# Optimization experiments

Hardware: AMD Instinct MI355X
Metric: run time of the kernel (lower is better)

## Reference

```python
import jax, jax.numpy as jnp
import numpy as np

NE, NM, D = 10000, 2048, 128
LEVELS = 6  # levels arg 5 -> self.levels = 6 relation types


def setup_inputs() -> dict:
    key = jax.random.key(0)
    ks = jax.random.split(key, 9)
    s = 0.05
    return {
        "emb_entity": jax.random.normal(ks[0], (1, NE, D), jnp.float32),
        "emb_mole": jax.random.normal(ks[1], (1, NM, D), jnp.float32),
        "entity_mole_weight": jax.random.uniform(ks[2], (NE, NM), jnp.float32),
        "W1": jax.random.normal(ks[3], (LEVELS, D, D), jnp.float32) * s,
        "root1": jax.random.normal(ks[4], (D, D), jnp.float32) * s,
        "b1": jax.random.normal(ks[5], (D,), jnp.float32) * s,
        "W2": jax.random.normal(ks[6], (LEVELS, D, D), jnp.float32) * s,
        "root2": jax.random.normal(ks[7], (D, D), jnp.float32) * s,
        "b2": jax.random.normal(ks[8], (D,), jnp.float32) * s,
    }


def reference(emb_entity, emb_mole, entity_mole_weight, W1, root1, b1, W2, root2, b2):
    x_e = emb_entity[0]  # [NE, D]
    x_m = emb_mole[0]    # [NM, D]
    # weight w in (i/LEVELS, (i+1)/LEVELS]  <=>  ceil(w*LEVELS) - 1 == i ; only i=1..LEVELS-1 form edges
    lev = jnp.ceil(entity_mole_weight * LEVELS).astype(jnp.int32) - 1  # [NE, NM]

    def rel_agg(x_src, W):
        # RGCN mean aggregation per relation type (edges Mole -> Entity), summed over relations
        out = jnp.zeros((x_e.shape[0], W.shape[-1]), x_src.dtype)
        for r in range(1, LEVELS):
            mask = (lev == r).astype(x_src.dtype)          # [NE, NM] relation-r adjacency
            cnt = mask.sum(axis=1, keepdims=True)          # in-degree per entity for relation r
            inv = jnp.where(cnt > 0, 1.0 / cnt, 0.0)
            out = out + ((mask @ x_src) * inv) @ W[r]      # mean message then relation transform
        return out

    # conv1 over homogeneous graph [Entity; Mole]; moles receive no edges -> root+bias only
    e1 = x_e @ root1 + rel_agg(x_m, W1) + b1
    m1 = x_m @ root1 + b1
    e1 = jax.nn.relu(e1)
    m1 = jax.nn.relu(m1)
    # conv2; only the entity slice of the output is returned
    e2 = e1 @ root2 + rel_agg(m1, W2) + b2
    return e2[None]  # [1, NE, D]
```

## Files before the change

### kernel.cpp

```cpp
#include <hip/hip_runtime.h>
#include <stdint.h>


#define NE 10000
#define NM 2048
#define NEPAD 10112
#define MB128 79
#define KSPLIT 16

typedef short bf8_t __attribute__((ext_vector_type(8)));
typedef float f16f  __attribute__((ext_vector_type(16)));

__device__ __forceinline__ uint16_t f2bf(float f){
  uint32_t u = __float_as_uint(f);
  u += 0x7FFFu + ((u >> 16) & 1u);
  return (uint16_t)(u >> 16);
}

__device__ __forceinline__ f16f mfma32(bf8_t a, bf8_t b, f16f c){
  return __builtin_amdgcn_mfma_f32_32x32x16_bf16(a, b, c, 0, 0, 0);
}

__global__ __launch_bounds__(256) void k_init(
    const float* __restrict__ root1, const float* __restrict__ root2,
    const float* __restrict__ W1, const float* __restrict__ W2,
    uint16_t* __restrict__ r1t, uint16_t* __restrict__ r2t,
    uint16_t* __restrict__ w1t, uint16_t* __restrict__ w2t,
    const float* __restrict__ w, const float* __restrict__ xe,
    uint32_t* __restrict__ levq, float* __restrict__ inv,
    uint16_t* __restrict__ xebf){
  int t = threadIdx.x;
  if (blockIdx.x < 48){
    int idx = blockIdx.x*4096 + t;
    #pragma unroll
    for (int it = 0; it < 16; it++, idx += 256){
      int slab = idx >> 14;
      int pos  = idx & 16383;
      int d = pos >> 7, k = pos & 127;
      float v; uint16_t* dst;
      if (slab == 0)      { v = root1[k*128 + d]; dst = r1t; }
      else if (slab == 1) { v = root2[k*128 + d]; dst = r2t; }
      else if (slab < 7)  { v = W1[(slab-1)*16384 + k*128 + d]; dst = w1t + (slab-2)*16384; }
      else                { v = W2[(slab-6)*16384 + k*128 + d]; dst = w2t + (slab-7)*16384; }
      dst[pos] = f2bf(v);
    }
    return;
  }
  int brow = (blockIdx.x - 48) * 32;
  int rloc = t >> 3, p = t & 7;
  int row = brow + rloc;
  bool active = row < NE;
  const float* wr = w + (size_t)row * NM;
  unsigned long long cnt = 0ull;
  __shared__ uint32_t tile[32][33];

  for (int cp = 0; cp < 8; cp++){
    uint32_t packs[4];
    #pragma unroll
    for (int q = 0; q < 4; q++){
      int gck = cp*32 + p + 8*q;
      uint32_t L = 0;
      if (active){
        const float4* f = (const float4*)(wr + gck*8);
        float4 f0 = f[0], f1 = f[1];
        float wv[8] = {f0.x,f0.y,f0.z,f0.w, f1.x,f1.y,f1.z,f1.w};
        #pragma unroll
        for (int e = 0; e < 8; e++){
          int s = (int)ceilf(wv[e]*6.0f);
          if (s >= 2) cnt += 1ull << (12*(s-2));
          L |= (uint32_t)s << (4*e);
        }
      }
      packs[q] = L;
    }
    __syncthreads();
    #pragma unroll
    for (int q = 0; q < 4; q++) tile[p + 8*q][rloc] = packs[q];
    __syncthreads();
    int ckk = t >> 3;
    int r4  = (t & 7) * 4;
    size_t base = (size_t)(cp*32 + ckk) * NEPAD + brow + r4;
    *(uint4*)(levq + base) = make_uint4(tile[ckk][r4], tile[ckk][r4+1],
                                        tile[ckk][r4+2], tile[ckk][r4+3]);
  }

  unsigned long long c = cnt;
  c += __shfl_xor(c, 1);
  c += __shfl_xor(c, 2);
  c += __shfl_xor(c, 4);
  if (p == 0 && row < NEPAD){
    if (active){
      inv[row*8 + 0] = 0.f; inv[row*8 + 6] = 0.f; inv[row*8 + 7] = 0.f;
      #pragma unroll
      for (int r = 1; r <= 5; r++){
        uint32_t cc = (uint32_t)((c >> (12*(r-1))) & 0xFFFull);
        inv[row*8 + r] = cc ? 1.0f/(float)cc : 0.f;
      }
    } else {
      #pragma unroll
      for (int i = 0; i < 8; i++) inv[row*8 + i] = 0.f;
    }
  }

  int f0i = p * 16;
  if (active){
    union { uint16_t u[16]; uint4 q[2]; } ub;
    #pragma unroll
    for (int j = 0; j < 4; j++){
      float4 a = *(const float4*)(xe + (size_t)row*128 + f0i + j*4);
      ub.u[j*4+0]=f2bf(a.x); ub.u[j*4+1]=f2bf(a.y); ub.u[j*4+2]=f2bf(a.z); ub.u[j*4+3]=f2bf(a.w);
    }
    *(uint4*)(xebf + (size_t)row*128 + f0i)     = ub.q[0];
    *(uint4*)(xebf + (size_t)row*128 + f0i + 8) = ub.q[1];
  } else if (row < NEPAD){
    uint4 z = make_uint4(0,0,0,0);
    *(uint4*)(xebf + (size_t)row*128 + f0i)     = z;
    *(uint4*)(xebf + (size_t)row*128 + f0i + 8) = z;
  }
}

__global__ __launch_bounds__(256) void k_gemm(
    const float* __restrict__ Af, const uint16_t* __restrict__ Bm,
    const uint16_t* __restrict__ Bz, const float* __restrict__ bias,
    uint16_t* __restrict__ m1out, uint16_t* __restrict__ zpk){
  int tid = threadIdx.x;
  int lane = tid & 63, wid = tid >> 6;
  int l31 = lane & 31, g = lane >> 5;
  int by = blockIdx.y;
  bool m1path = (by == 0);
  int r = by - 1;
  const uint16_t* B = m1path ? Bm : (Bz + (size_t)r*16384);
  int arow = blockIdx.x*128 + wid*32 + l31;

  f16f acc[4];
  #pragma unroll
  for (int n = 0; n < 4; n++)
    #pragma unroll
    for (int i = 0; i < 16; i++) acc[n][i] = 0.f;

  #pragma unroll
  for (int ksI = 0; ksI < 8; ksI++){
    int k0 = ksI*16 + g*8;
    const float* ap = Af + (size_t)arow*128 + k0;
    float4 f0 = *(const float4*)ap;
    float4 f1 = *(const float4*)(ap + 4);
    union { uint16_t u[8]; bf8_t v; } ua;
    ua.u[0]=f2bf(f0.x); ua.u[1]=f2bf(f0.y); ua.u[2]=f2bf(f0.z); ua.u[3]=f2bf(f0.w);
    ua.u[4]=f2bf(f1.x); ua.u[5]=f2bf(f1.y); ua.u[6]=f2bf(f1.z); ua.u[7]=f2bf(f1.w);
    #pragma unroll
    for (int n = 0; n < 4; n++){
      bf8_t b = *(const bf8_t*)(B + (size_t)(n*32 + l31)*128 + k0);
      acc[n] = mfma32(ua.v, b, acc[n]);
    }
  }
  #pragma unroll
  for (int n = 0; n < 4; n++){
    int colg = n*32 + l31;
    float bv = m1path ? bias[colg] : 0.f;
    #pragma unroll
    for (int v = 0; v < 16; v++){
      int rowl = (v&3) + 8*(v>>2) + 4*g;
      int rg = blockIdx.x*128 + wid*32 + rowl;
      float val = acc[n][v];
      if (m1path){
        m1out[(size_t)rg*128 + colg] = f2bf(fmaxf(val + bv, 0.f));
      } else {
        int pos = ((rg & 1) << 2) | ((rg & 7) >> 1);
        zpk[(size_t)(r*256 + (rg>>3))*1024 + colg*8 + pos] = f2bf(val);
      }
    }
  }
}

template<int NSLAB, bool FUSE>
__global__ __launch_bounds__(256, 2) void k_conv(
    const uint32_t* __restrict__ levq, const float* __restrict__ inv,
    const uint16_t* __restrict__ zpk, const uint16_t* __restrict__ aroot,
    const uint16_t* __restrict__ rt,
    const uint16_t* __restrict__ gA, const uint16_t* __restrict__ gB,
    uint16_t* __restrict__ gOut,
    uint16_t* __restrict__ p16, float* __restrict__ p32){
  int tid = threadIdx.x;
  int lane = tid & 63, wid = tid >> 6;
  int l31 = lane & 31, g = lane >> 5;

  if (FUSE && blockIdx.x >= MB128){
    int b = blockIdx.y*5 + (blockIdx.x - MB128);
    int r = b >> 4;
    int rowb = (b & 15)*128 + wid*32;
    int arow = rowb + l31;
    const uint16_t* B = gB + (size_t)r*16384;
    f16f acc[4];
    #pragma unroll
    for (int n = 0; n < 4; n++)
      #pragma unroll
      for (int i = 0; i < 16; i++) acc[n][i] = 0.f;
    #pragma unroll
    for (int ksI = 0; ksI < 8; ksI++){
      int k0 = ksI*16 + g*8;
      bf8_t a = *(const bf8_t*)(gA + (size_t)arow*128 + k0);
      #pragma unroll
      for (int n = 0; n < 4; n++){
        bf8_t bb = *(const bf8_t*)(B + (size_t)(n*32 + l31)*128 + k0);
        acc[n] = mfma32(a, bb, acc[n]);
      }
    }
    #pragma unroll
    for (int n = 0; n < 4; n++){
      int colg = n*32 + l31;
      #pragma unroll
      for (int v = 0; v < 16; v++){
        int rowl = (v&3) + 8*(v>>2) + 4*g;
        int rg = rowb + rowl;
        int pos = ((rg & 1) << 2) | ((rg & 7) >> 1);
        gOut[(size_t)(r*256 + (rg>>3))*1024 + colg*8 + pos] = f2bf(acc[n][v]);
      }
    }
    return;
  }

  int wm = wid >> 1, wn = wid & 1;
  int brow = blockIdx.x*128;
  int ks = blockIdx.y;
  int kc0 = ks*16;
  int rowA = brow + wm*64 + l31;
  int rowB = rowA + 32;
  int colb = wn*64;

  uint32_t LA[8], LB[8];
  #pragma unroll
  for (int kk = 0; kk < 8; kk++){
    int kt = kc0 + kk*2 + g;
    LA[kk] = levq[(size_t)kt*NEPAD + rowA];
    LB[kk] = levq[(size_t)kt*NEPAD + rowB];
  }

  uint32_t tlo[2][5], thi[2][5];
  #pragma unroll
  for (int mt = 0; mt < 2; mt++){
    int rg = mt ? rowB : rowA;
    #pragma unroll
    for (int r = 1; r <= 5; r++){
      uint32_t bits = (uint32_t)f2bf(inv[(size_t)rg*8 + r]);
      int sh = 8*((r+1)&3);
      tlo[mt][r-1] = (bits & 0xFFu) << sh;
      thi[mt][r-1] = (bits >> 8)    << sh;
    }
  }

  f16f acc[2][2];
  #pragma unroll
  for (int a0=0;a0<2;a0++)
    #pragma unroll
    for (int b0=0;b0<2;b0++)
      #pragma unroll
      for (int i=0;i<16;i++) acc[a0][b0][i]=0.f;

  if (ks < 8){
    int k0 = ks*16 + g*8;
    bf8_t a0 = *(const bf8_t*)(aroot + (size_t)rowA*128 + k0);
    bf8_t a1 = *(const bf8_t*)(aroot + (size_t)rowB*128 + k0);
    #pragma unroll
    for (int nt = 0; nt < 2; nt++){
      bf8_t rb = *(const bf8_t*)(rt + (size_t)(colb + nt*32 + l31)*128 + k0);
      acc[0][nt] = mfma32(a0, rb, acc[0][nt]);
      acc[1][nt] = mfma32(a1, rb, acc[1][nt]);
    }
  }

  #pragma unroll
  for (int kk = 0; kk < 8; kk++){
    int kt = kc0 + kk*2 + g;
    uint32_t sxA = LA[kk] & 0x0F0F0F0Fu, syA = (LA[kk] >> 4) & 0x0F0F0F0Fu;
    uint32_t sxB = LB[kk] & 0x0F0F0F0Fu, syB = (LB[kk] >> 4) & 0x0F0F0F0Fu;
    const uint16_t* zb = zpk + (size_t)kt*1024 + (size_t)(colb + l31)*8;
    #pragma unroll
    for (int r = 1; r <= 5; r++){
      const uint16_t* zr = zb + (size_t)(r-1)*262144;
      bf8_t bn0 = *(const bf8_t*)(zr);
      bf8_t bn1 = *(const bf8_t*)(zr + 256);
      #pragma unroll
      for (int mt = 0; mt < 2; mt++){
        uint32_t sx = mt ? sxB : sxA;
        uint32_t sy = mt ? syB : syA;
        uint32_t TL = tlo[mt][r-1], TH = thi[mt][r-1];
        uint32_t pl, ph, ql, qh;
        if (r < 3){
          pl = __builtin_amdgcn_perm(0u, TL, sx);
          ph = __builtin_amdgcn_perm(0u, TH, sx);
          ql = __builtin_amdgcn_perm(0u, TL, sy);
          qh = __builtin_amdgcn_perm(0u, TH, sy);
        } else {
          pl = __builtin_amdgcn_perm(TL, 0u, sx);
          ph = __builtin_amdgcn_perm(TH, 0u, sx);
          ql = __builtin_amdgcn_perm(TL, 0u, sy);
          qh = __builtin_amdgcn_perm(TH, 0u, sy);
        }
        union { uint32_t u[4]; bf8_t v; } A;
        A.u[0] = __builtin_amdgcn_perm(ph, pl, 0x05010400u);
        A.u[1] = __builtin_amdgcn_perm(ph, pl, 0x07030602u);
        A.u[2] = __builtin_amdgcn_perm(qh, ql, 0x05010400u);
        A.u[3] = __builtin_amdgcn_perm(qh, ql, 0x07030602u);
        acc[mt][0] = mfma32(A.v, bn0, acc[mt][0]);
        acc[mt][1] = mfma32(A.v, bn1, acc[mt][1]);
      }
    }
  }

  if (NSLAB == KSPLIT){
    uint16_t* dst = p16 + (size_t)ks*NEPAD*128;
    #pragma unroll
    for (int mt = 0; mt < 2; mt++){
      #pragma unroll
      for (int nt = 0; nt < 2; nt++){
        int colg = colb + nt*32 + l31;
        #pragma unroll
        for (int v = 0; v < 16; v++){
          int rowl = (v&3) + 8*(v>>2) + 4*g;
          dst[(size_t)(brow + wm*64 + mt*32 + rowl)*128 + colg] = f2bf(acc[mt][nt][v]);
        }
      }
    }
  } else {
    #pragma unroll
    for (int mt = 0; mt < 2; mt++){
      #pragma unroll
      for (int nt = 0; nt < 2; nt++){
        int colg = colb + nt*32 + l31;
        #pragma unroll
        for (int v = 0; v < 16; v++){
          int rowl = (v&3) + 8*(v>>2) + 4*g;
          unsafeAtomicAdd(&p32[(size_t)(brow + wm*64 + mt*32 + rowl)*128 + colg],
                          acc[mt][nt][v]);
        }
      }
    }
  }
}

template<bool C1, bool S16>
__global__ __launch_bounds__(256) void k_red(
    const uint16_t* __restrict__ p16, const float* __restrict__ p32,
    const float* __restrict__ bias, uint16_t* __restrict__ e1bf,
    float* __restrict__ out){
  size_t idx8 = ((size_t)blockIdx.x*256 + threadIdx.x) * 8;
  int col = (int)(idx8 & 127);
  float s[8];
  #pragma unroll
  for (int j = 0; j < 8; j++) s[j] = bias[col + j];
  if (S16){
    #pragma unroll
    for (int sl = 0; sl < KSPLIT; sl++){
      union { uint4 q; uint16_t h[8]; } u;
      u.q = *(const uint4*)(p16 + (size_t)sl*NEPAD*128 + idx8);
      #pragma unroll
      for (int j = 0; j < 8; j++) s[j] += __uint_as_float(((uint32_t)u.h[j]) << 16);
    }
  } else {
    #pragma unroll
    for (int j = 0; j < 8; j += 4){
      float4 v = *(const float4*)(p32 + idx8 + j);
      s[j] += v.x; s[j+1] += v.y; s[j+2] += v.z; s[j+3] += v.w;
    }
  }
  if (C1){
    union { uint16_t u[8]; uint4 q; } ub;
    #pragma unroll
    for (int j = 0; j < 8; j++) ub.u[j] = f2bf(fmaxf(s[j], 0.f));
    *(uint4*)(e1bf + idx8) = ub.q;
  } else {
    if (idx8 < (size_t)NE*128){
      *(float4*)(out + idx8)     = make_float4(s[0], s[1], s[2], s[3]);
      *(float4*)(out + idx8 + 4) = make_float4(s[4], s[5], s[6], s[7]);
    }
  }
}

extern "C" void kernel_launch(void* const* d_in, const int* in_sizes, int n_in,
                              void* d_out, int out_size, void* d_ws, size_t ws_size,
                              hipStream_t stream){
  const float* xe  = (const float*)d_in[0];
  const float* xm  = (const float*)d_in[1];
  const float* w   = (const float*)d_in[2];
  const float* W1  = (const float*)d_in[3];
  const float* r1  = (const float*)d_in[4];
  const float* b1  = (const float*)d_in[5];
  const float* W2  = (const float*)d_in[6];
  const float* r2  = (const float*)d_in[7];
  const float* b2  = (const float*)d_in[8];
  float* out = (float*)d_out;
  char* ws = (char*)d_ws;

  constexpr size_t OFF_INV  = 0;
  constexpr size_t OFF_XEBF = OFF_INV  + (size_t)NEPAD*8*4;
  constexpr size_t OFF_M1   = OFF_XEBF + (size_t)NEPAD*128*2;
  constexpr size_t OFF_Z1   = OFF_M1   + (size_t)NM*128*2;
  constexpr size_t OFF_Z2   = OFF_Z1   + (size_t)5*NM*128*2;
  constexpr size_t OFF_R1T  = OFF_Z2   + (size_t)5*NM*128*2;
  constexpr size_t OFF_R2T  = OFF_R1T  + 128*128*2;
  constexpr size_t OFF_W1T  = OFF_R2T  + 128*128*2;
  constexpr size_t OFF_W2T  = OFF_W1T  + (size_t)5*128*128*2;
  constexpr size_t OFF_LEVQ = OFF_W2T  + (size_t)5*128*128*2;
  constexpr size_t OFF_PART = OFF_LEVQ + (size_t)256*NEPAD*4;
  constexpr size_t SLAB16   = (size_t)NEPAD*128*2;
  constexpr size_t NEED_A   = OFF_PART + (size_t)KSPLIT*SLAB16;
  constexpr size_t SLABF    = (size_t)NEPAD*128*4;

  float*    inv  = (float*)   (ws + OFF_INV);
  uint16_t* xebf = (uint16_t*)(ws + OFF_XEBF);
  uint16_t* m1   = (uint16_t*)(ws + OFF_M1);
  uint16_t* z1   = (uint16_t*)(ws + OFF_Z1);
  uint16_t* z2   = (uint16_t*)(ws + OFF_Z2);
  uint16_t* r1t  = (uint16_t*)(ws + OFF_R1T);
  uint16_t* r2t  = (uint16_t*)(ws + OFF_R2T);
  uint16_t* w1t  = (uint16_t*)(ws + OFF_W1T);
  uint16_t* w2t  = (uint16_t*)(ws + OFF_W2T);
  uint32_t* levq = (uint32_t*)(ws + OFF_LEVQ);
  uint16_t* p16  = (uint16_t*)(ws + OFF_PART);
  float*    p32  = (float*)   (ws + OFF_PART);

  bool tierA = (ws_size >= NEED_A);

  hipLaunchKernelGGL(k_init, dim3(48 + NEPAD/32), dim3(256), 0, stream,
                     r1, r2, W1, W2, r1t, r2t, w1t, w2t,
                     w, xe, levq, inv, xebf);
  hipLaunchKernelGGL(k_gemm, dim3(16,6), dim3(256), 0, stream,
                     xm, r1t, w1t, b1, m1, z1);
  if (tierA){
    hipLaunchKernelGGL((k_conv<KSPLIT,true>), dim3(MB128 + 5, KSPLIT), dim3(256), 0,
                       stream, levq, inv, z1, xebf, r1t, m1, w2t, z2,
                       p16, (float*)nullptr);
    hipLaunchKernelGGL((k_red<true,true>), dim3(NEPAD*128/2048), dim3(256), 0, stream,
                       p16, (const float*)nullptr, b1, xebf, (float*)nullptr);
    hipLaunchKernelGGL((k_conv<KSPLIT,false>), dim3(MB128, KSPLIT), dim3(256), 0, stream,
                       levq, inv, z2, xebf, r2t,
                       (const uint16_t*)nullptr, (const uint16_t*)nullptr,
                       (uint16_t*)nullptr, p16, (float*)nullptr);
    hipLaunchKernelGGL((k_red<false,true>), dim3(NEPAD*128/2048), dim3(256), 0, stream,
                       p16, (const float*)nullptr, b2, (uint16_t*)nullptr, out);
  } else {
    hipMemsetAsync(p32, 0, SLABF, stream);
    hipLaunchKernelGGL((k_conv<1,true>), dim3(MB128 + 5, KSPLIT), dim3(256), 0, stream,
                       levq, inv, z1, xebf, r1t, m1, w2t, z2,
                       (uint16_t*)nullptr, p32);
    hipLaunchKernelGGL((k_red<true,false>), dim3(NEPAD*128/2048), dim3(256), 0, stream,
                       (const uint16_t*)nullptr, p32, b1, xebf, (float*)nullptr);
    hipMemsetAsync(p32, 0, SLABF, stream);
    hipLaunchKernelGGL((k_conv<1,false>), dim3(MB128, KSPLIT), dim3(256), 0, stream,
                       levq, inv, z2, xebf, r2t,
                       (const uint16_t*)nullptr, (const uint16_t*)nullptr,
                       (uint16_t*)nullptr, (uint16_t*)nullptr, p32);
    hipLaunchKernelGGL((k_red<false,false>), dim3(NEPAD*128/2048), dim3(256), 0, stream,
                       (const uint16_t*)nullptr, p32, b2, (uint16_t*)nullptr, out);
  }
}
```

Before: 125.2 us.

## Fuse conv1 reduction and root2 GEMM into conv2 kernel, stagger k-order

Removes the separate conv1 reduction kernel. Conv2's aggregation no longer depends on e1, so its aggregation blocks run alongside extra blocks that reduce the conv1 partials, apply ReLU and compute e1@root2 into an fp32 slab; a final reduction adds everything. This is meant to save one launch and the serialization point. The k-slice traversal is also rotated by block index to spread memory accesses, and occupancy is raised to 3 blocks per SM. The cost is extra workspace for separate partial buffers and a root slab, plus 34KB of LDS in the conv2 kernel, which may limit occupancy.

```diff
diff --git a/kernel.cpp b/kernel.cpp
--- a/kernel.cpp
+++ b/kernel.cpp
@@ -172,55 +172,18 @@
   }
 }
 
-template<int NSLAB, bool FUSE>
-__global__ __launch_bounds__(256, 2) void k_conv(
+template<bool S16, bool ROOT>
+__device__ __forceinline__ void conv_core(
     const uint32_t* __restrict__ levq, const float* __restrict__ inv,
     const uint16_t* __restrict__ zpk, const uint16_t* __restrict__ aroot,
     const uint16_t* __restrict__ rt,
-    const uint16_t* __restrict__ gA, const uint16_t* __restrict__ gB,
-    uint16_t* __restrict__ gOut,
-    uint16_t* __restrict__ p16, float* __restrict__ p32){
-  int tid = threadIdx.x;
+    uint16_t* __restrict__ p16, float* __restrict__ p32,
+    int tid){
   int lane = tid & 63, wid = tid >> 6;
   int l31 = lane & 31, g = lane >> 5;
-
-  if (FUSE && blockIdx.x >= MB128){
-    int b = blockIdx.y*5 + (blockIdx.x - MB128);
-    int r = b >> 4;
-    int rowb = (b & 15)*128 + wid*32;
-    int arow = rowb + l31;
-    const uint16_t* B = gB + (size_t)r*16384;
-    f16f acc[4];
-    #pragma unroll
-    for (int n = 0; n < 4; n++)
-      #pragma unroll
-      for (int i = 0; i < 16; i++) acc[n][i] = 0.f;
-    #pragma unroll
-    for (int ksI = 0; ksI < 8; ksI++){
-      int k0 = ksI*16 + g*8;
-      bf8_t a = *(const bf8_t*)(gA + (size_t)arow*128 + k0);
-      #pragma unroll
-      for (int n = 0; n < 4; n++){
-        bf8_t bb = *(const bf8_t*)(B + (size_t)(n*32 + l31)*128 + k0);
-        acc[n] = mfma32(a, bb, acc[n]);
-      }
-    }
-    #pragma unroll
-    for (int n = 0; n < 4; n++){
-      int colg = n*32 + l31;
-      #pragma unroll
-      for (int v = 0; v < 16; v++){
-        int rowl = (v&3) + 8*(v>>2) + 4*g;
-        int rg = rowb + rowl;
-        int pos = ((rg & 1) << 2) | ((rg & 7) >> 1);
-        gOut[(size_t)(r*256 + (rg>>3))*1024 + colg*8 + pos] = f2bf(acc[n][v]);
-      }
-    }
-    return;
-  }
-
   int wm = wid >> 1, wn = wid & 1;
-  int brow = blockIdx.x*128;
+  int bx = blockIdx.x;
+  int brow = bx*128;
   int ks = blockIdx.y;
   int kc0 = ks*16;
   int rowA = brow + wm*64 + l31;
@@ -229,10 +192,10 @@
 
   uint32_t LA[8], LB[8];
   #pragma unroll
-  for (int kk = 0; kk < 8; kk++){
-    int kt = kc0 + kk*2 + g;
-    LA[kk] = levq[(size_t)kt*NEPAD + rowA];
-    LB[kk] = levq[(size_t)kt*NEPAD + rowB];
+  for (int j = 0; j < 8; j++){
+    int kt = kc0 + ((j + bx) & 7)*2 + g;
+    LA[j] = levq[(size_t)kt*NEPAD + rowA];
+    LB[j] = levq[(size_t)kt*NEPAD + rowB];
   }
 
   uint32_t tlo[2][5], thi[2][5];
@@ -256,7 +219,7 @@
       #pragma unroll
       for (int i=0;i<16;i++) acc[a0][b0][i]=0.f;
 
-  if (ks < 8){
+  if (ROOT && ks < 8){
     int k0 = ks*16 + g*8;
     bf8_t a0 = *(const bf8_t*)(aroot + (size_t)rowA*128 + k0);
     bf8_t a1 = *(const bf8_t*)(aroot + (size_t)rowB*128 + k0);
@@ -270,7 +233,7 @@
 
   #pragma unroll
   for (int kk = 0; kk < 8; kk++){
-    int kt = kc0 + kk*2 + g;
+    int kt = kc0 + ((kk + bx) & 7)*2 + g;
     uint32_t sxA = LA[kk] & 0x0F0F0F0Fu, syA = (LA[kk] >> 4) & 0x0F0F0F0Fu;
     uint32_t sxB = LB[kk] & 0x0F0F0F0Fu, syB = (LB[kk] >> 4) & 0x0F0F0F0Fu;
     const uint16_t* zb = zpk + (size_t)kt*1024 + (size_t)(colb + l31)*8;
@@ -307,7 +270,7 @@
     }
   }
 
-  if (NSLAB == KSPLIT){
+  if (S16){
     uint16_t* dst = p16 + (size_t)ks*NEPAD*128;
     #pragma unroll
     for (int mt = 0; mt < 2; mt++){
@@ -338,42 +301,166 @@
   }
 }
 
-template<bool C1, bool S16>
-__global__ __launch_bounds__(256) void k_red(
-    const uint16_t* __restrict__ p16, const float* __restrict__ p32,
-    const float* __restrict__ bias, uint16_t* __restrict__ e1bf,
+template<bool S16>
+__global__ __launch_bounds__(256, 3) void k_convA(
+    const uint32_t* __restrict__ levq, const float* __restrict__ inv,
+    const uint16_t* __restrict__ zpk, const uint16_t* __restrict__ aroot,
+    const uint16_t* __restrict__ rt,
+    const uint16_t* __restrict__ gA, const uint16_t* __restrict__ gB,
+    uint16_t* __restrict__ gOut,
+    uint16_t* __restrict__ p16, float* __restrict__ p32){
+  int tid = threadIdx.x;
+  int lane = tid & 63, wid = tid >> 6;
+  int l31 = lane & 31, g = lane >> 5;
+
+  if (blockIdx.x >= MB128){
+    int b = blockIdx.y*5 + (blockIdx.x - MB128);
+    int r = b >> 4;
+    int rowb = (b & 15)*128 + wid*32;
+    int arow = rowb + l31;
+    const uint16_t* B = gB + (size_t)r*16384;
+    f16f acc[4];
+    #pragma unroll
+    for (int n = 0; n < 4; n++)
+      #pragma unroll
+      for (int i = 0; i < 16; i++) acc[n][i] = 0.f;
+    #pragma unroll
+    for (int ksI = 0; ksI < 8; ksI++){
+      int k0 = ksI*16 + g*8;
+      bf8_t a = *(const bf8_t*)(gA + (size_t)arow*128 + k0);
+      #pragma unroll
+      for (int n = 0; n < 4; n++){
+        bf8_t bb = *(const bf8_t*)(B + (size_t)(n*32 + l31)*128 + k0);
+        acc[n] = mfma32(a, bb, acc[n]);
+      }
+    }
+    #pragma unroll
+    for (int n = 0; n < 4; n++){
+      int colg = n*32 + l31;
+      #pragma unroll
+      for (int v = 0; v < 16; v++){
+        int rowl = (v&3) + 8*(v>>2) + 4*g;
+        int rg = rowb + rowl;
+        int pos = ((rg & 1) << 2) | ((rg & 7) >> 1);
+        gOut[(size_t)(r*256 + (rg>>3))*1024 + colg*8 + pos] = f2bf(acc[n][v]);
+      }
+    }
+    return;
+  }
+  conv_core<S16, true>(levq, inv, zpk, aroot, rt, p16, p32, tid);
+}
+
+template<bool S16>
+__global__ __launch_bounds__(256, 3) void k_convB(
+    const uint32_t* __restrict__ levq, const float* __restrict__ inv,
+    const uint16_t* __restrict__ zpk,
+    const uint16_t* __restrict__ pA16, const float* __restrict__ pA32,
+    const uint16_t* __restrict__ rt, const float* __restrict__ b1,
+    uint16_t* __restrict__ pB16, float* __restrict__ pB32,
+    float* __restrict__ rootslab){
+  __shared__ uint16_t e1s[128*136];
+  int tid = threadIdx.x;
+  int lane = tid & 63, wid = tid >> 6;
+  int l31 = lane & 31, g = lane >> 5;
+
+  if (blockIdx.x >= MB128){
+    int rid = blockIdx.y*5 + (blockIdx.x - MB128);
+    if (rid >= MB128) return;
+    #pragma unroll
+    for (int c = 0; c < 8; c++){
+      int eo = c*2048 + tid*8;
+      size_t base = (size_t)rid*16384 + eo;
+      int col = eo & 127;
+      float s[8];
+      float4 bv0 = *(const float4*)(b1 + col);
+      float4 bv1 = *(const float4*)(b1 + col + 4);
+      s[0]=bv0.x; s[1]=bv0.y; s[2]=bv0.z; s[3]=bv0.w;
+      s[4]=bv1.x; s[5]=bv1.y; s[6]=bv1.z; s[7]=bv1.w;
+      if (S16){
+        #pragma unroll
+        for (int sl = 0; sl < KSPLIT; sl++){
+          union { uint4 q; uint16_t h[8]; } u;
+          u.q = *(const uint4*)(pA16 + (size_t)sl*NEPAD*128 + base);
+          #pragma unroll
+          for (int j = 0; j < 8; j++) s[j] += __uint_as_float(((uint32_t)u.h[j]) << 16);
+        }
+      } else {
+        #pragma unroll
+        for (int j = 0; j < 8; j += 4){
+          float4 v = *(const float4*)(pA32 + base + j);
+          s[j] += v.x; s[j+1] += v.y; s[j+2] += v.z; s[j+3] += v.w;
+        }
+      }
+      union { uint16_t u[8]; uint4 q; } ub;
+      #pragma unroll
+      for (int j = 0; j < 8; j++) ub.u[j] = f2bf(fmaxf(s[j], 0.f));
+      int row = eo >> 7;
+      *(uint4*)(&e1s[row*136 + col]) = ub.q;
+    }
+    __syncthreads();
+    f16f racc[4];
+    #pragma unroll
+    for (int n = 0; n < 4; n++)
+      #pragma unroll
+      for (int i = 0; i < 16; i++) racc[n][i] = 0.f;
+    #pragma unroll
+    for (int kk = 0; kk < 8; kk++){
+      int k0 = kk*16 + g*8;
+      bf8_t a = *(const bf8_t*)(&e1s[(wid*32 + l31)*136 + k0]);
+      #pragma unroll
+      for (int n = 0; n < 4; n++){
+        bf8_t b = *(const bf8_t*)(rt + (size_t)(n*32 + l31)*128 + k0);
+        racc[n] = mfma32(a, b, racc[n]);
+      }
+    }
+    #pragma unroll
+    for (int n = 0; n < 4; n++){
+      int colg = n*32 + l31;
+      #pragma unroll
+      for (int v = 0; v < 16; v++){
+        int rowl = (v&3) + 8*(v>>2) + 4*g;
+        rootslab[(size_t)(rid*128 + wid*32 + rowl)*128 + colg] = racc[n][v];
+      }
+    }
+    return;
+  }
+  conv_core<S16, false>(levq, inv, zpk, (const uint16_t*)nullptr, rt, pB16, pB32, tid);
+}
+
+template<bool S16>
+__global__ __launch_bounds__(256) void k_red2(
+    const uint16_t* __restrict__ pB16, const float* __restrict__ pB32,
+    const float* __restrict__ rootslab, const float* __restrict__ b2,
     float* __restrict__ out){
   size_t idx8 = ((size_t)blockIdx.x*256 + threadIdx.x) * 8;
+  if (idx8 >= (size_t)NE*128) return;
   int col = (int)(idx8 & 127);
   float s[8];
-  #pragma unroll
-  for (int j = 0; j < 8; j++) s[j] = bias[col + j];
+  float4 bv0 = *(const float4*)(b2 + col);
+  float4 bv1 = *(const float4*)(b2 + col + 4);
+  s[0]=bv0.x; s[1]=bv0.y; s[2]=bv0.z; s[3]=bv0.w;
+  s[4]=bv1.x; s[5]=bv1.y; s[6]=bv1.z; s[7]=bv1.w;
+  float4 r0 = *(const float4*)(rootslab + idx8);
+  float4 r1 = *(const float4*)(rootslab + idx8 + 4);
+  s[0]+=r0.x; s[1]+=r0.y; s[2]+=r0.z; s[3]+=r0.w;
+  s[4]+=r1.x; s[5]+=r1.y; s[6]+=r1.z; s[7]+=r1.w;
   if (S16){
     #pragma unroll
     for (int sl = 0; sl < KSPLIT; sl++){
       union { uint4 q; uint16_t h[8]; } u;
-      u.q = *(const uint4*)(p16 + (size_t)sl*NEPAD*128 + idx8);
+      u.q = *(const uint4*)(pB16 + (size_t)sl*NEPAD*128 + idx8);
       #pragma unroll
       for (int j = 0; j < 8; j++) s[j] += __uint_as_float(((uint32_t)u.h[j]) << 16);
     }
   } else {
     #pragma unroll
     for (int j = 0; j < 8; j += 4){
-      float4 v = *(const float4*)(p32 + idx8 + j);
+      float4 v = *(const float4*)(pB32 + idx8 + j);
       s[j] += v.x; s[j+1] += v.y; s[j+2] += v.z; s[j+3] += v.w;
     }
   }
-  if (C1){
-    union { uint16_t u[8]; uint4 q; } ub;
-    #pragma unroll
-    for (int j = 0; j < 8; j++) ub.u[j] = f2bf(fmaxf(s[j], 0.f));
-    *(uint4*)(e1bf + idx8) = ub.q;
-  } else {
-    if (idx8 < (size_t)NE*128){
-      *(float4*)(out + idx8)     = make_float4(s[0], s[1], s[2], s[3]);
-      *(float4*)(out + idx8 + 4) = make_float4(s[4], s[5], s[6], s[7]);
-    }
-  }
+  *(float4*)(out + idx8)     = make_float4(s[0], s[1], s[2], s[3]);
+  *(float4*)(out + idx8 + 4) = make_float4(s[4], s[5], s[6], s[7]);
 }
 
 extern "C" void kernel_launch(void* const* d_in, const int* in_sizes, int n_in,
@@ -401,10 +488,15 @@
   constexpr size_t OFF_W1T  = OFF_R2T  + 128*128*2;
   constexpr size_t OFF_W2T  = OFF_W1T  + (size_t)5*128*128*2;
   constexpr size_t OFF_LEVQ = OFF_W2T  + (size_t)5*128*128*2;
-  constexpr size_t OFF_PART = OFF_LEVQ + (size_t)256*NEPAD*4;
+  constexpr size_t OFF_PA   = OFF_LEVQ + (size_t)256*NEPAD*4;
   constexpr size_t SLAB16   = (size_t)NEPAD*128*2;
-  constexpr size_t NEED_A   = OFF_PART + (size_t)KSPLIT*SLAB16;
   constexpr size_t SLABF    = (size_t)NEPAD*128*4;
+  constexpr size_t OFF_PB   = OFF_PA   + (size_t)KSPLIT*SLAB16;
+  constexpr size_t OFF_ROOT = OFF_PB   + (size_t)KSPLIT*SLAB16;
+  constexpr size_t NEED_A   = OFF_ROOT + SLABF;
+  constexpr size_t OFF_PB_B   = OFF_PA + SLABF;
+  constexpr size_t OFF_ROOT_B = OFF_PB_B + SLABF;
+  constexpr size_t NEED_B     = OFF_ROOT_B + SLABF;
 
   float*    inv  = (float*)   (ws + OFF_INV);
   uint16_t* xebf = (uint16_t*)(ws + OFF_XEBF);
@@ -416,8 +508,6 @@
   uint16_t* w1t  = (uint16_t*)(ws + OFF_W1T);
   uint16_t* w2t  = (uint16_t*)(ws + OFF_W2T);
   uint32_t* levq = (uint32_t*)(ws + OFF_LEVQ);
-  uint16_t* p16  = (uint16_t*)(ws + OFF_PART);
-  float*    p32  = (float*)   (ws + OFF_PART);
 
   bool tierA = (ws_size >= NEED_A);
 
@@ -427,30 +517,30 @@
   hipLaunchKernelGGL(k_gemm, dim3(16,6), dim3(256), 0, stream,
                      xm, r1t, w1t, b1, m1, z1);
   if (tierA){
-    hipLaunchKernelGGL((k_conv<KSPLIT,true>), dim3(MB128 + 5, KSPLIT), dim3(256), 0,
-                       stream, levq, inv, z1, xebf, r1t, m1, w2t, z2,
-                       p16, (float*)nullptr);
-    hipLaunchKernelGGL((k_red<true,true>), dim3(NEPAD*128/2048), dim3(256), 0, stream,
-                       p16, (const float*)nullptr, b1, xebf, (float*)nullptr);
-    hipLaunchKernelGGL((k_conv<KSPLIT,false>), dim3(MB128, KSPLIT), dim3(256), 0, stream,
-                       levq, inv, z2, xebf, r2t,
-                       (const uint16_t*)nullptr, (const uint16_t*)nullptr,
-                       (uint16_t*)nullptr, p16, (float*)nullptr);
-    hipLaunchKernelGGL((k_red<false,true>), dim3(NEPAD*128/2048), dim3(256), 0, stream,
-                       p16, (const float*)nullptr, b2, (uint16_t*)nullptr, out);
+    uint16_t* pA   = (uint16_t*)(ws + OFF_PA);
+    uint16_t* pB   = (uint16_t*)(ws + OFF_PB);
+    float*    root = (float*)   (ws + OFF_ROOT);
+    hipLaunchKernelGGL((k_convA<true>), dim3(MB128 + 5, KSPLIT), dim3(256), 0, stream,
+                       levq, inv, z1, xebf, r1t, m1, w2t, z2,
+                       pA, (float*)nullptr);
+    hipLaunchKernelGGL((k_convB<true>), dim3(MB128 + 5, KSPLIT), dim3(256), 0, stream,
+                       levq, inv, z2, pA, (const float*)nullptr, r2t, b1,
+                       pB, (float*)nullptr, root);
+    hipLaunchKernelGGL((k_red2<true>), dim3((NE*128 + 2047)/2048), dim3(256), 0, stream,
+                       pB, (const float*)nullptr, root, b2, out);
   } else {
-    hipMemsetAsync(p32, 0, SLABF, stream);
-    hipLaunchKernelGGL((k_conv<1,true>), dim3(MB128 + 5, KSPLIT), dim3(256), 0, stream,
+    float* pA   = (float*)(ws + OFF_PA);
+    float* pB   = (float*)(ws + OFF_PB_B);
+    float* root = (float*)(ws + OFF_ROOT_B);
+    hipMemsetAsync(pA, 0, SLABF, stream);
+    hipMemsetAsync(pB, 0, SLABF, stream);
+    hipLaunchKernelGGL((k_convA<false>), dim3(MB128 + 5, KSPLIT), dim3(256), 0, stream,
                        levq, inv, z1, xebf, r1t, m1, w2t, z2,
-                       (uint16_t*)nullptr, p32);
-    hipLaunchKernelGGL((k_red<true,false>), dim3(NEPAD*128/2048), dim3(256), 0, stream,
-                       (const uint16_t*)nullptr, p32, b1, xebf, (float*)nullptr);
-    hipMemsetAsync(p32, 0, SLABF, stream);
-    hipLaunchKernelGGL((k_conv<1,false>), dim3(MB128, KSPLIT), dim3(256), 0, stream,
-                       levq, inv, z2, xebf, r2t,
-                       (const uint16_t*)nullptr, (const uint16_t*)nullptr,
-                       (uint16_t*)nullptr, (uint16_t*)nullptr, p32);
-    hipLaunchKernelGGL((k_red<false,false>), dim3(NEPAD*128/2048), dim3(256), 0, stream,
-                       (const uint16_t*)nullptr, p32, b2, (uint16_t*)nullptr, out);
-  }
-}
+                       (uint16_t*)nullptr, pA);
+    hipLaunchKernelGGL((k_convB<false>), dim3(MB128 + 5, KSPLIT), dim3(256), 0, stream,
+                       levq, inv, z2, (const uint16_t*)nullptr, pA, r2t, b1,
+                       (uint16_t*)nullptr, pB, root);
+    hipLaunchKernelGGL((k_red2<false>), dim3((NE*128 + 2047)/2048), dim3(256), 0, stream,
+                       (const uint16_t*)nullptr, pB, root, b2, out);
+  }
+}
```

After: 127.9 us. +2.2%, slower.
